# Kernel optimization log

Measured on AMD Instinct MI355X. Metric: run time of the kernel, lower is better.

Reference implementation:

```python
import jax, jax.numpy as jnp
import numpy as np

# Model config (matches init_kwargs)
D_MODEL = 1536
NUM_HEADS = 16
QUERY_GROUPS = 4
HEAD_DIM = D_MODEL // NUM_HEADS  # 96
HEADS_PER_GROUP = NUM_HEADS // QUERY_GROUPS
ROPE_THETA = 10000.0
B, T, GH, GW = 2, 16, 16, 16
S = GH * GW  # spatial patches per frame
QKV_OUT = NUM_HEADS * HEAD_DIM + 2 * QUERY_GROUPS * HEAD_DIM  # 2304


def setup_inputs() -> dict:
    key = jax.random.key(0)
    k1, k2, k3 = jax.random.split(key, 3)
    x = jax.random.normal(k1, (B, T, S, D_MODEL), dtype=jnp.float32)
    padding_mask = jnp.ones((B * T, S), dtype=jnp.int32)
    # nn.Linear weights stored as [out, in]; y = x @ W.T
    w_qkv = jax.random.normal(k2, (QKV_OUT, D_MODEL), dtype=jnp.float32) * (1.0 / np.sqrt(D_MODEL))
    w_o = jax.random.normal(k3, (D_MODEL, D_MODEL), dtype=jnp.float32) * (1.0 / np.sqrt(D_MODEL))
    return {"x": x, "padding_mask": padding_mask, "w_qkv": w_qkv, "w_o": w_o}


def _rot_half(seg, cos, sin):
    # seg: [..., d]; half-split rotary rotation
    d = seg.shape[-1] // 2
    x1, x2 = seg[..., :d], seg[..., d:]
    return jnp.concatenate([x1 * cos - x2 * sin, x1 * sin + x2 * cos], axis=-1)


def _cos_sin(pos, seg_dim):
    # pos: [L] -> cos/sin [L, seg_dim//2]
    inv_freq = 1.0 / (ROPE_THETA ** (jnp.arange(seg_dim // 2, dtype=jnp.float32) * 2.0 / seg_dim))
    ang = pos.astype(jnp.float32)[:, None] * inv_freq[None, :]
    return jnp.cos(ang), jnp.sin(ang)


def _apply_rope3d(x):
    # x: [B*T, S, heads, HEAD_DIM]; head_dim split equally over (t, h, w) axes
    seg = HEAD_DIM // 3  # 32
    t_pos = jnp.tile(jnp.arange(T), B)            # [B*T] temporal index per attention-batch row
    h_pos = jnp.repeat(jnp.arange(GH), GW)        # [S]
    w_pos = jnp.tile(jnp.arange(GW), GH)          # [S]
    ct, st = _cos_sin(t_pos, seg)  # [B*T, seg/2]
    ch, sh = _cos_sin(h_pos, seg)  # [S, seg/2]
    cw, sw = _cos_sin(w_pos, seg)
    xt = _rot_half(x[..., :seg], ct[:, None, None, :], st[:, None, None, :])
    xh = _rot_half(x[..., seg:2 * seg], ch[None, :, None, :], sh[None, :, None, :])
    xw = _rot_half(x[..., 2 * seg:], cw[None, :, None, :], sw[None, :, None, :])
    return jnp.concatenate([xt, xh, xw], axis=-1)


def reference(x, padding_mask, w_qkv, w_o):
    # Spatial attention mode: [B, T, S, D] -> [B*T, S, D]
    xs = x.reshape(B * T, S, D_MODEL)
    qkv = jnp.einsum('bsd,od->bso', xs, w_qkv)  # [B*T, S, QKV_OUT]
    q_end = NUM_HEADS * HEAD_DIM
    k_end = q_end + QUERY_GROUPS * HEAD_DIM
    q = qkv[..., :q_end].reshape(B * T, S, NUM_HEADS, HEAD_DIM)
    k = qkv[..., q_end:k_end].reshape(B * T, S, QUERY_GROUPS, HEAD_DIM)
    v = qkv[..., k_end:].reshape(B * T, S, QUERY_GROUPS, HEAD_DIM)
    # RoPE3D on q and k
    q = _apply_rope3d(q)
    k = _apply_rope3d(k)
    # GQA: extend kv heads to num_heads (repeat_interleave)
    k = jnp.repeat(k, HEADS_PER_GROUP, axis=2)  # [B*T, S, NUM_HEADS, HEAD_DIM]
    v = jnp.repeat(v, HEADS_PER_GROUP, axis=2)
    scale = 1.0 / np.sqrt(HEAD_DIM)
    scores = jnp.einsum('bqhd,bkhd->bhqk', q, k) * scale  # [B*T, H, S, S]
    mask = (padding_mask != 0)[:, None, None, :]  # [B*T, 1, 1, S], True = attend
    scores = jnp.where(mask, scores, jnp.float32(-1e9))
    probs = jax.nn.softmax(scores, axis=-1)
    attn = jnp.einsum('bhqk,bkhd->bqhd', probs, v).reshape(B * T, S, D_MODEL)
    out = jnp.einsum('bsd,od->bso', attn, w_o)
    return out.reshape(B, T, S, D_MODEL)
```

## Files before the change

kernel.cpp:

```cpp
#include <hip/hip_runtime.h>
#include <hip/hip_bf16.h>
#include <stdint.h>

typedef __attribute__((ext_vector_type(8))) short short8;
typedef __attribute__((ext_vector_type(4))) float f32x4;
typedef __attribute__((ext_vector_type(4))) float f4;
typedef __attribute__((ext_vector_type(4))) short s4;

typedef __attribute__((address_space(1))) const void gvoid_t;
typedef __attribute__((address_space(3))) void lvoid_t;

__device__ __forceinline__ void gload_lds16(const void* g, void* l) {
  __builtin_amdgcn_global_load_lds((gvoid_t*)g, (lvoid_t*)l, 16, 0, 0);
}

__device__ __forceinline__ ushort f2b(float f) {
  union { float f; uint32_t u; } v; v.f = f;
  return (ushort)((v.u + 0x7fffu + ((v.u >> 16) & 1u)) >> 16);
}
__device__ __forceinline__ float b2f(ushort b) {
  union { uint32_t u; float f; } v; v.u = ((uint32_t)b) << 16;
  return v.f;
}

template <int N> __device__ __forceinline__ void wait_vmcnt();
template <> __device__ __forceinline__ void wait_vmcnt<0>() { asm volatile("s_waitcnt vmcnt(0)" ::: "memory"); }

__device__ __forceinline__ void wait_lgkm0() {
  asm volatile("s_waitcnt lgkmcnt(0)" ::: "memory");
  __builtin_amdgcn_sched_barrier(0);
}
__device__ __forceinline__ void barrier_fence() {
  asm volatile("s_barrier" ::: "memory");
}

__global__ void prep_kernel(const float* __restrict__ x, const float* __restrict__ wq,
                            const float* __restrict__ wo,
                            ushort* __restrict__ Xb, ushort* __restrict__ Wq,
                            ushort* __restrict__ Wo, float2* __restrict__ tab) {
  int b = blockIdx.x, tid = threadIdx.x;
  const float* in; ushort* out; int i;
  if (b < 12288)      { in = x;  out = Xb; i = b * 256 + tid; }
  else if (b < 15744) { in = wq; out = Wq; i = (b - 12288) * 256 + tid; }
  else if (b < 18048) { in = wo; out = Wo; i = (b - 15744) * 256 + tid; }
  else {
    int pos = tid >> 4, fi = tid & 15;
    float inv_freq = __expf(-(float)fi * 0.5756462732485115f);
    float ang = (float)pos * inv_freq;
    float sn, c;
    __sincosf(ang, &sn, &c);
    tab[tid] = make_float2(c, sn);
    return;
  }
  f4 v = ((const f4*)in)[i];
  s4 o;
  o.x = (short)f2b(v.x); o.y = (short)f2b(v.y);
  o.z = (short)f2b(v.z); o.w = (short)f2b(v.w);
  ((s4*)out)[i] = o;
}

template <int BN, typename OutT>
__global__ __launch_bounds__(512, 2) void gemm6(const ushort* __restrict__ A,
                                                const ushort* __restrict__ B,
                                                OutT* __restrict__ C,
                                                int N, int K) {
  constexpr int NF = BN / 32;
  constexpr int RB = BN / 2;
  constexpr int ABUF = 256 * 64;
  constexpr int BBUF = BN * 64;
  constexpr uint ABYTE = ABUF * 2;
  constexpr uint BBYTE = BBUF * 2;
  constexpr int BRND = BN / 64;
  constexpr int BTW = (BN % 64) / 8;

  __shared__ ushort As[2 * ABUF];
  __shared__ ushort Bs[2 * BBUF];

  const int tid = threadIdx.x;
  const int l = tid & 63, w = tid >> 6;
  const int wr = w >> 1, wc = w & 1;
  const int r16 = l & 15, kh = l >> 4;
  const int sc = (l & 7) ^ (l >> 3);
  const int srow = w * 8 + (l >> 3);

  const int xcd = blockIdx.x & 7;
  const int ii = blockIdx.x >> 3;
  const int bm = xcd * 4 + (ii & 3);
  const int bn = ii >> 2;
  const ushort* Ag = A + (size_t)bm * 256 * K;
  const ushort* Bg = B + (size_t)bn * BN * K;
  const int NT = K >> 6;

  const char* AsR = (const char*)As;
  const char* BsR = (const char*)Bs;
  const uint khsw = ((uint)kh * 16) ^ ((uint)(r16 & 7) * 16);
  const uint PA = (uint)(wr * 64 + r16) * 128 + khsw;
  const uint PB = (uint)(wc * RB + r16) * 128 + khsw;

  const ushort* ga[4];
  const ushort* gb[BRND];
  const ushort* gbt = nullptr;
#pragma unroll
  for (int i = 0; i < 4; ++i) ga[i] = Ag + (size_t)(i * 64 + srow) * K + sc * 8;
#pragma unroll
  for (int i = 0; i < BRND; ++i) gb[i] = Bg + (size_t)(i * 64 + srow) * K + sc * 8;
  if constexpr (BTW > 0) gbt = Bg + (size_t)(BRND * 64 + srow) * K + sc * 8;

#pragma unroll
  for (int i = 0; i < 4; ++i) gload_lds16(ga[i], As + i * 4096 + w * 512);
#pragma unroll
  for (int i = 0; i < BRND; ++i) gload_lds16(gb[i], Bs + i * 4096 + w * 512);
  if constexpr (BTW > 0) { if (w < BTW) gload_lds16(gbt, Bs + BRND * 4096 + w * 512); }
#pragma unroll
  for (int i = 0; i < 4; ++i) ga[i] += 64;
#pragma unroll
  for (int i = 0; i < BRND; ++i) gb[i] += 64;
  if constexpr (BTW > 0) gbt += 64;
  wait_vmcnt<0>();
  barrier_fence();

  f32x4 acc[4][NF] = {};
  short8 afr[4], bfr[NF];

  for (int u = 0; u < NT; ++u) {
    const int cur = u & 1;
    const uint aoff = cur ? ABYTE : 0u;
    const uint boff = cur ? BBYTE : 0u;
    ushort* An = As + (cur ^ 1) * ABUF;
    ushort* Bn = Bs + (cur ^ 1) * BBUF;
    const bool st = (u + 1 < NT);

    {
      const uint pa = PA + aoff, pb = PB + boff;
#pragma unroll
      for (int m = 0; m < 4; ++m) afr[m] = *(const short8*)(AsR + pa + m * 2048);
#pragma unroll
      for (int n = 0; n < NF; ++n) bfr[n] = *(const short8*)(BsR + pb + n * 2048);
    }
    if (st) {
#pragma unroll
      for (int i = 0; i < 4; ++i) gload_lds16(ga[i], An + i * 4096 + w * 512);
    }
    wait_lgkm0();
    __builtin_amdgcn_s_setprio(1);
#pragma unroll
    for (int m = 0; m < 4; ++m)
#pragma unroll
      for (int n = 0; n < NF; ++n)
        acc[m][n] = __builtin_amdgcn_mfma_f32_16x16x32_bf16(afr[m], bfr[n], acc[m][n], 0, 0, 0);
    __builtin_amdgcn_s_setprio(0);

    {
      const uint pa = (PA ^ 64u) + aoff, pb = (PB ^ 64u) + boff;
#pragma unroll
      for (int m = 0; m < 4; ++m) afr[m] = *(const short8*)(AsR + pa + m * 2048);
#pragma unroll
      for (int n = 0; n < NF; ++n) bfr[n] = *(const short8*)(BsR + pb + n * 2048);
    }
    if (st) {
#pragma unroll
      for (int i = 0; i < BRND; ++i) gload_lds16(gb[i], Bn + i * 4096 + w * 512);
      if constexpr (BTW > 0) { if (w < BTW) gload_lds16(gbt, Bn + BRND * 4096 + w * 512); }
    }
    wait_lgkm0();
    __builtin_amdgcn_s_setprio(1);
#pragma unroll
    for (int m = 0; m < 4; ++m)
#pragma unroll
      for (int n = 0; n < NF; ++n)
        acc[m][n] = __builtin_amdgcn_mfma_f32_16x16x32_bf16(afr[m], bfr[n], acc[m][n], 0, 0, 0);
    __builtin_amdgcn_s_setprio(0);

#pragma unroll
    for (int i = 0; i < 4; ++i) ga[i] += 64;
#pragma unroll
    for (int i = 0; i < BRND; ++i) gb[i] += 64;
    if constexpr (BTW > 0) gbt += 64;
    wait_vmcnt<0>();
    barrier_fence();
  }

  const int rowb = bm * 256 + wr * 64;
  const int colb = bn * BN + wc * RB;
#pragma unroll
  for (int m = 0; m < 4; ++m)
#pragma unroll
    for (int n = 0; n < NF; ++n)
#pragma unroll
      for (int r = 0; r < 4; ++r) {
        int row = rowb + m * 16 + kh * 4 + r;
        int col = colb + n * 16 + r16;
        float val = acc[m][n][r];
        if constexpr (sizeof(OutT) == 2) C[(size_t)row * N + col] = f2b(val);
        else                             C[(size_t)row * N + col] = val;
      }
}

template <int BN, int KC, typename OutT>
__global__ __launch_bounds__(256, 2) void gemm12(const ushort* __restrict__ A,
                                                 const ushort* __restrict__ B,
                                                 OutT* __restrict__ C) {
  constexpr int NF = BN / 32;
  constexpr int RB = BN / 2;
  constexpr int ABUF = 128 * 64;
  constexpr int BBUF = BN * 64;
  constexpr uint ABYTE = ABUF * 2;
  constexpr uint BBYTE = BBUF * 2;
  constexpr int ARND = 4;
  constexpr int BRND = BN / 32;
  constexpr int NT = KC >> 6;

  __shared__ ushort As[2 * ABUF];
  __shared__ ushort Bs[2 * BBUF];

  const int tid = threadIdx.x;
  const int l = tid & 63, w = tid >> 6;
  const int wr = w >> 1, wc = w & 1;
  const int r16 = l & 15, kh = l >> 4;
  const int sc = (l & 7) ^ (l >> 3);
  const int srow = w * 8 + (l >> 3);

  const int xcd = blockIdx.x & 7;
  const int ii = blockIdx.x >> 3;
  const int bm = xcd * 8 + (ii & 7);
  const int bn = ii >> 3;
  const ushort* Ag = A + (size_t)bm * 128 * KC;
  const ushort* Bg = B + (size_t)bn * BN * KC;

  const char* AsR = (const char*)As;
  const char* BsR = (const char*)Bs;
  const uint khsw = ((uint)kh * 16) ^ ((uint)(r16 & 7) * 16);
  const uint PA = (uint)(wr * 64 + r16) * 128 + khsw;
  const uint PB = (uint)(wc * RB + r16) * 128 + khsw;

  const ushort* gA = Ag + (size_t)srow * KC + sc * 8;
  const ushort* gB = Bg + (size_t)srow * KC + sc * 8;

#pragma unroll
  for (int i = 0; i < ARND; ++i) gload_lds16(gA + (size_t)(i * 32) * KC, As + i * 2048 + w * 512);
#pragma unroll
  for (int i = 0; i < BRND; ++i) gload_lds16(gB + (size_t)(i * 32) * KC, Bs + i * 2048 + w * 512);
  gA += 64; gB += 64;
  wait_vmcnt<0>();
  barrier_fence();

  f32x4 acc[4][NF] = {};
  short8 afr[4], bfr[NF];

  for (int u = 0; u < NT; ++u) {
    const int cur = u & 1;
    const uint aoff = cur ? ABYTE : 0u;
    const uint boff = cur ? BBYTE : 0u;
    ushort* An = As + (cur ^ 1) * ABUF;
    ushort* Bn = Bs + (cur ^ 1) * BBUF;
    const bool st = (u + 1 < NT);

    {
      const uint pa = PA + aoff, pb = PB + boff;
#pragma unroll
      for (int m = 0; m < 4; ++m) afr[m] = *(const short8*)(AsR + pa + m * 2048);
#pragma unroll
      for (int n = 0; n < NF; ++n) bfr[n] = *(const short8*)(BsR + pb + n * 2048);
    }
    if (st) {
#pragma unroll
      for (int i = 0; i < ARND; ++i) gload_lds16(gA + (size_t)(i * 32) * KC, An + i * 2048 + w * 512);
    }
    wait_lgkm0();
    __builtin_amdgcn_s_setprio(1);
#pragma unroll
    for (int m = 0; m < 4; ++m)
#pragma unroll
      for (int n = 0; n < NF; ++n)
        acc[m][n] = __builtin_amdgcn_mfma_f32_16x16x32_bf16(afr[m], bfr[n], acc[m][n], 0, 0, 0);
    __builtin_amdgcn_s_setprio(0);

    {
      const uint pa = (PA ^ 64u) + aoff, pb = (PB ^ 64u) + boff;
#pragma unroll
      for (int m = 0; m < 4; ++m) afr[m] = *(const short8*)(AsR + pa + m * 2048);
#pragma unroll
      for (int n = 0; n < NF; ++n) bfr[n] = *(const short8*)(BsR + pb + n * 2048);
    }
    if (st) {
#pragma unroll
      for (int i = 0; i < BRND; ++i) gload_lds16(gB + (size_t)(i * 32) * KC, Bn + i * 2048 + w * 512);
    }
    wait_lgkm0();
    __builtin_amdgcn_s_setprio(1);
#pragma unroll
    for (int m = 0; m < 4; ++m)
#pragma unroll
      for (int n = 0; n < NF; ++n)
        acc[m][n] = __builtin_amdgcn_mfma_f32_16x16x32_bf16(afr[m], bfr[n], acc[m][n], 0, 0, 0);
    __builtin_amdgcn_s_setprio(0);

    gA += 64; gB += 64;
    wait_vmcnt<0>();
    barrier_fence();
  }

  const int rowb = bm * 128 + wr * 64;
  const int colb = bn * BN + wc * RB;
#pragma unroll
  for (int m = 0; m < 4; ++m)
#pragma unroll
    for (int n = 0; n < NF; ++n)
#pragma unroll
      for (int r = 0; r < 4; ++r) {
        int row = rowb + m * 16 + kh * 4 + r;
        int col = colb + n * 16 + r16;
        float val = acc[m][n][r];
        if constexpr (sizeof(OutT) == 2) C[(size_t)row * (BN * 8) + col] = f2b(val);
        else                             C[(size_t)row * (BN * 8) + col] = val;
      }
}

__device__ __forceinline__ short8 shfl_xor32(short8 v) {
  union { short8 s; int i[4]; } a, b;
  a.s = v;
#pragma unroll
  for (int q = 0; q < 4; ++q) b.i[q] = __shfl_xor(a.i[q], 32, 64);
  return b.s;
}
__device__ __forceinline__ short8 rope_frag(short8 v, int pos, int kh, const float2* Tb) {
  short8 p = shfl_xor32(v);
  const float sgn = (kh < 2) ? -1.0f : 1.0f;
  const int ib = pos * 16 + (kh & 1) * 8;
  short8 o;
#pragma unroll
  for (int j = 0; j < 8; ++j) {
    float2 cs = Tb[ib + j];
    o[j] = (short)f2b(b2f((ushort)v[j]) * cs.x + sgn * b2f((ushort)p[j]) * cs.y);
  }
  return o;
}

__global__ __launch_bounds__(512, 1) void attn3_kernel(
    const ushort* __restrict__ QKV,
    const int* __restrict__ mask,
    const float2* __restrict__ Tab,
    ushort* __restrict__ Out) {
  __shared__ ushort Ks[256 * 104];
  __shared__ ushort Vs[96 * 264];
  __shared__ ushort Ps[8][16 * 136];
  __shared__ float Mb[256];
  __shared__ float2 Tb[256];

  const int b = blockIdx.x;
  const int qt = b & 1;
  const int g = (b >> 1) & 3;
  const int bt = b >> 3;
  const int t = threadIdx.x;
  const int l = t & 63, w = t >> 6;
  const int r16 = l & 15, kh = l >> 4;
  const int h = g * 4 + (w >> 1);
  const int qc = w & 1;
  const int t0 = bt & 15;

  if (t < 256) { Tb[t] = Tab[t]; Mb[t] = mask[bt * 256 + t] ? 0.0f : -1.0e9f; }
  __syncthreads();

  {
    const int r = t >> 1, ch = t & 1;
    const ushort* src = QKV + (size_t)(bt * 256 + r) * 2304 + 1536 + g * 96;
    const int p1 = r >> 4, p2 = r & 15;
    if (ch == 0) {
      short8 v0 = *(const short8*)(src + 0);
      short8 v1 = *(const short8*)(src + 8);
      short8 v2 = *(const short8*)(src + 16);
      short8 v3 = *(const short8*)(src + 24);
      short8 o0, o1, o2, o3;
#pragma unroll
      for (int j = 0; j < 8; ++j) {
        float2 ca = Tb[t0 * 16 + j], cb = Tb[t0 * 16 + 8 + j];
        float x1a = b2f((ushort)v0[j]), x2a = b2f((ushort)v2[j]);
        float x1b = b2f((ushort)v1[j]), x2b = b2f((ushort)v3[j]);
        o0[j] = (short)f2b(x1a * ca.x - x2a * ca.y);
        o1[j] = (short)f2b(x1b * cb.x - x2b * cb.y);
        o2[j] = (short)f2b(x1a * ca.y + x2a * ca.x);
        o3[j] = (short)f2b(x1b * cb.y + x2b * cb.x);
      }
      *(short8*)(&Ks[r * 104 + 0])  = o0;
      *(short8*)(&Ks[r * 104 + 8])  = o1;
      *(short8*)(&Ks[r * 104 + 16]) = o2;
      *(short8*)(&Ks[r * 104 + 24]) = o3;
      v0 = *(const short8*)(src + 32);
      v1 = *(const short8*)(src + 40);
      v2 = *(const short8*)(src + 48);
      v3 = *(const short8*)(src + 56);
#pragma unroll
      for (int j = 0; j < 8; ++j) {
        float2 ca = Tb[p1 * 16 + j], cb = Tb[p1 * 16 + 8 + j];
        float x1a = b2f((ushort)v0[j]), x2a = b2f((ushort)v2[j]);
        float x1b = b2f((ushort)v1[j]), x2b = b2f((ushort)v3[j]);
        o0[j] = (short)f2b(x1a * ca.x - x2a * ca.y);
        o1[j] = (short)f2b(x1b * cb.x - x2b * cb.y);
        o2[j] = (short)f2b(x1a * ca.y + x2a * ca.x);
        o3[j] = (short)f2b(x1b * cb.y + x2b * cb.x);
      }
      *(short8*)(&Ks[r * 104 + 32]) = o0;
      *(short8*)(&Ks[r * 104 + 40]) = o1;
      *(short8*)(&Ks[r * 104 + 48]) = o2;
      *(short8*)(&Ks[r * 104 + 56]) = o3;
    } else {
      short8 v0 = *(const short8*)(src + 64);
      short8 v1 = *(const short8*)(src + 72);
      short8 v2 = *(const short8*)(src + 80);
      short8 v3 = *(const short8*)(src + 88);
      short8 o0, o1, o2, o3;
#pragma unroll
      for (int j = 0; j < 8; ++j) {
        float2 ca = Tb[p2 * 16 + j], cb = Tb[p2 * 16 + 8 + j];
        float x1a = b2f((ushort)v0[j]), x2a = b2f((ushort)v2[j]);
        float x1b = b2f((ushort)v1[j]), x2b = b2f((ushort)v3[j]);
        o0[j] = (short)f2b(x1a * ca.x - x2a * ca.y);
        o1[j] = (short)f2b(x1b * cb.x - x2b * cb.y);
        o2[j] = (short)f2b(x1a * ca.y + x2a * ca.x);
        o3[j] = (short)f2b(x1b * cb.y + x2b * cb.x);
      }
      *(short8*)(&Ks[r * 104 + 64]) = o0;
      *(short8*)(&Ks[r * 104 + 72]) = o1;
      *(short8*)(&Ks[r * 104 + 80]) = o2;
      *(short8*)(&Ks[r * 104 + 88]) = o3;
    }
  }

#pragma unroll
  for (int i = 0; i < 6; ++i) {
    int c = t + i * 512;
    int s = c / 12, dq = c - s * 12;
    short8 vv = *(const short8*)(QKV + (size_t)(bt * 256 + s) * 2304 + 1920 + g * 96 + dq * 8);
#pragma unroll
    for (int j = 0; j < 8; ++j)
      Vs[(dq * 8 + j) * 264 + s] = (ushort)vv[j];
  }
  __syncthreads();

  const ushort* Qp = QKV + (size_t)(bt * 256 + qt * 128 + qc * 64) * 2304 + h * 96;
  ushort* Pw = &Ps[w][0];
  const float scale = 0.10206207261596575f;

#pragma unroll
  for (int mp = 0; mp < 2; ++mp) {
    const int qb = mp * 32;
    const int p1A = qt * 8 + qc * 4 + mp * 2;
    const int p1B = p1A + 1;

    short8 qfA[3], qfB[3];
    {
      short8 rA0 = *(const short8*)(Qp + (size_t)(qb + r16) * 2304 + 0 + kh * 8);
      short8 rA1 = *(const short8*)(Qp + (size_t)(qb + r16) * 2304 + 32 + kh * 8);
      short8 rA2 = *(const short8*)(Qp + (size_t)(qb + r16) * 2304 + 64 + kh * 8);
      short8 rB0 = *(const short8*)(Qp + (size_t)(qb + 16 + r16) * 2304 + 0 + kh * 8);
      short8 rB1 = *(const short8*)(Qp + (size_t)(qb + 16 + r16) * 2304 + 32 + kh * 8);
      short8 rB2 = *(const short8*)(Qp + (size_t)(qb + 16 + r16) * 2304 + 64 + kh * 8);
      qfA[0] = rope_frag(rA0, t0, kh, Tb);
      qfA[1] = rope_frag(rA1, p1A, kh, Tb);
      qfA[2] = rope_frag(rA2, r16, kh, Tb);
      qfB[0] = rope_frag(rB0, t0, kh, Tb);
      qfB[1] = rope_frag(rB1, p1B, kh, Tb);
      qfB[2] = rope_frag(rB2, r16, kh, Tb);
    }

    f32x4 scA[16] = {}, scB[16] = {};
#pragma unroll
    for (int f = 0; f < 16; ++f) {
#pragma unroll
      for (int kc = 0; kc < 3; ++kc) {
        short8 kf = *(const short8*)(&Ks[(f * 16 + r16) * 104 + kc * 32 + kh * 8]);
        scA[f] = __builtin_amdgcn_mfma_f32_16x16x32_bf16(qfA[kc], kf, scA[f], 0, 0, 0);
        scB[f] = __builtin_amdgcn_mfma_f32_16x16x32_bf16(qfB[kc], kf, scB[f], 0, 0, 0);
      }
    }

#pragma unroll
    for (int f = 0; f < 16; ++f) {
      float mb = Mb[f * 16 + r16];
#pragma unroll
      for (int r = 0; r < 4; ++r) {
        scA[f][r] = scA[f][r] * scale + mb;
        scB[f][r] = scB[f][r] * scale + mb;
      }
    }

    float invA[4], invB[4];
#pragma unroll
    for (int reg = 0; reg < 4; ++reg) {
      float mxA = -3.0e38f, mxB = -3.0e38f;
#pragma unroll
      for (int f = 0; f < 16; ++f) { mxA = fmaxf(mxA, scA[f][reg]); mxB = fmaxf(mxB, scB[f][reg]); }
      for (int o = 8; o >= 1; o >>= 1) { mxA = fmaxf(mxA, __shfl_xor(mxA, o, 64)); mxB = fmaxf(mxB, __shfl_xor(mxB, o, 64)); }
      float smA = 0.f, smB = 0.f;
#pragma unroll
      for (int f = 0; f < 16; ++f) {
        float pA = __expf(scA[f][reg] - mxA);
        float pB = __expf(scB[f][reg] - mxB);
        scA[f][reg] = pA; scB[f][reg] = pB;
        smA += pA; smB += pB;
      }
      for (int o = 8; o >= 1; o >>= 1) { smA += __shfl_xor(smA, o, 64); smB += __shfl_xor(smB, o, 64); }
      invA[reg] = 1.0f / smA;
      invB[reg] = 1.0f / smB;
    }

    short8 pfA[8], pfB[8];
#pragma unroll
    for (int ck = 0; ck < 2; ++ck) {
#pragma unroll
      for (int f = 0; f < 8; ++f)
#pragma unroll
        for (int reg = 0; reg < 4; ++reg)
          Pw[(kh * 4 + reg) * 136 + f * 16 + r16] = f2b(scA[ck * 8 + f][reg]);
#pragma unroll
      for (int kc = 0; kc < 4; ++kc)
        pfA[ck * 4 + kc] = *(const short8*)(&Pw[r16 * 136 + kc * 32 + kh * 8]);
    }
#pragma unroll
    for (int ck = 0; ck < 2; ++ck) {
#pragma unroll
      for (int f = 0; f < 8; ++f)
#pragma unroll
        for (int reg = 0; reg < 4; ++reg)
          Pw[(kh * 4 + reg) * 136 + f * 16 + r16] = f2b(scB[ck * 8 + f][reg]);
#pragma unroll
      for (int kc = 0; kc < 4; ++kc)
        pfB[ck * 4 + kc] = *(const short8*)(&Pw[r16 * 136 + kc * 32 + kh * 8]);
    }

    f32x4 oA[6] = {}, oB[6] = {};
#pragma unroll
    for (int dt = 0; dt < 6; ++dt) {
#pragma unroll
      for (int kc = 0; kc < 8; ++kc) {
        short8 vf = *(const short8*)(&Vs[(dt * 16 + r16) * 264 + kc * 32 + kh * 8]);
        oA[dt] = __builtin_amdgcn_mfma_f32_16x16x32_bf16(pfA[kc], vf, oA[dt], 0, 0, 0);
        oB[dt] = __builtin_amdgcn_mfma_f32_16x16x32_bf16(pfB[kc], vf, oB[dt], 0, 0, 0);
      }
    }

    const int rbase = bt * 256 + qt * 128 + qc * 64 + qb;
#pragma unroll
    for (int dt = 0; dt < 6; ++dt)
#pragma unroll
      for (int reg = 0; reg < 4; ++reg) {
        int col = h * 96 + dt * 16 + r16;
        Out[(size_t)(rbase + kh * 4 + reg) * 1536 + col]      = f2b(oA[dt][reg] * invA[reg]);
        Out[(size_t)(rbase + 16 + kh * 4 + reg) * 1536 + col] = f2b(oB[dt][reg] * invB[reg]);
      }
  }
}

extern "C" void kernel_launch(void* const* d_in, const int* in_sizes, int n_in,
                              void* d_out, int out_size, void* d_ws, size_t ws_size,
                              hipStream_t stream) {
  const float* x     = (const float*)d_in[0];
  const int* pmask   = (const int*)d_in[1];
  const float* w_qkv = (const float*)d_in[2];
  const float* w_o   = (const float*)d_in[3];
  float* out = (float*)d_out;

  char* ws = (char*)d_ws;
  ushort* Xb  = (ushort*)(ws + 0);
  ushort* Wq  = (ushort*)(ws + 25165824);
  ushort* Wo  = (ushort*)(ws + 32243712);
  ushort* QKV = (ushort*)(ws + 36962304);
  float2* Tab = (float2*)(ws + 74711040);
  ushort* Attn = Xb;

  prep_kernel<<<18049, 256, 0, stream>>>(x, w_qkv, w_o, Xb, Wq, Wo, Tab);

  gemm6<288, ushort><<<256, 512, 0, stream>>>(Xb, Wq, QKV, 2304, 1536);

  attn3_kernel<<<256, 512, 0, stream>>>(QKV, pmask, Tab, Attn);

  gemm12<192, 1536, float><<<512, 256, 0, stream>>>(Attn, Wo, out);
}
```

Measured before the change: 147.5 us.

## Fuse fp32-to-bf16 conversion of x into the QKV GEMM's A-tile loads

The QKV projection GEMM now reads the fp32 activations directly, converts them to bf16 in registers with packed conversion instructions, and writes them to LDS. This replaces the separate pass that wrote a bf16 copy of x. The goal is to remove the extra read and write of the 25 MB activation buffer, at the cost of register-staged A loads instead of async global-to-LDS loads. Separately, the output projection switches from gemm12 to gemm6 with BN=192 and 512-thread blocks, and the workspace layout is rearranged.

```diff
diff --git a/kernel.cpp b/kernel.cpp
--- a/kernel.cpp
+++ b/kernel.cpp
@@ -6,6 +6,7 @@
 typedef __attribute__((ext_vector_type(4))) float f32x4;
 typedef __attribute__((ext_vector_type(4))) float f4;
 typedef __attribute__((ext_vector_type(4))) short s4;
+typedef __attribute__((ext_vector_type(4))) uint u4;
 
 typedef __attribute__((address_space(1))) const void gvoid_t;
 typedef __attribute__((address_space(3))) void lvoid_t;
@@ -22,6 +23,11 @@
   union { uint32_t u; float f; } v; v.u = ((uint32_t)b) << 16;
   return v.f;
 }
+__device__ __forceinline__ uint cvtpk(float lo, float hi) {
+  uint r;
+  asm volatile("v_cvt_pk_bf16_f32 %0, %1, %2" : "=v"(r) : "v"(lo), "v"(hi));
+  return r;
+}
 
 template <int N> __device__ __forceinline__ void wait_vmcnt();
 template <> __device__ __forceinline__ void wait_vmcnt<0>() { asm volatile("s_waitcnt vmcnt(0)" ::: "memory"); }
@@ -34,15 +40,13 @@
   asm volatile("s_barrier" ::: "memory");
 }
 
-__global__ void prep_kernel(const float* __restrict__ x, const float* __restrict__ wq,
-                            const float* __restrict__ wo,
-                            ushort* __restrict__ Xb, ushort* __restrict__ Wq,
-                            ushort* __restrict__ Wo, float2* __restrict__ tab) {
+__global__ void prep2_kernel(const float* __restrict__ wq, const float* __restrict__ wo,
+                             ushort* __restrict__ Wq, ushort* __restrict__ Wo,
+                             float2* __restrict__ tab) {
   int b = blockIdx.x, tid = threadIdx.x;
   const float* in; ushort* out; int i;
-  if (b < 12288)      { in = x;  out = Xb; i = b * 256 + tid; }
-  else if (b < 15744) { in = wq; out = Wq; i = (b - 12288) * 256 + tid; }
-  else if (b < 18048) { in = wo; out = Wo; i = (b - 15744) * 256 + tid; }
+  if (b < 3456)      { in = wq; out = Wq; i = b * 256 + tid; }
+  else if (b < 5760) { in = wo; out = Wo; i = (b - 3456) * 256 + tid; }
   else {
     int pos = tid >> 4, fi = tid & 15;
     float inv_freq = __expf(-(float)fi * 0.5756462732485115f);
@@ -57,6 +61,165 @@
   o.x = (short)f2b(v.x); o.y = (short)f2b(v.y);
   o.z = (short)f2b(v.z); o.w = (short)f2b(v.w);
   ((s4*)out)[i] = o;
+}
+
+__global__ __launch_bounds__(512, 2) void gemm6x(const float* __restrict__ Af,
+                                                 const ushort* __restrict__ B,
+                                                 ushort* __restrict__ C) {
+  constexpr int BN = 288, NF = 9, RB = 144;
+  constexpr int K = 1536, NT = 24;
+  constexpr int ABUF = 256 * 64;
+  constexpr int BBUF = BN * 64;
+  constexpr uint ABYTE = ABUF * 2;
+  constexpr uint BBYTE = BBUF * 2;
+  constexpr int BRND = 4, BTW = 4;
+
+  __shared__ ushort As[2 * ABUF];
+  __shared__ ushort Bs[2 * BBUF];
+
+  const int tid = threadIdx.x;
+  const int l = tid & 63, w = tid >> 6;
+  const int wr = w >> 1, wc = w & 1;
+  const int r16 = l & 15, kh = l >> 4;
+  const int sc = (l & 7) ^ (l >> 3);
+  const int srow = w * 8 + (l >> 3);
+
+  const int xcd = blockIdx.x & 7;
+  const int ii = blockIdx.x >> 3;
+  const int bm = xcd * 4 + (ii & 3);
+  const int bn = ii >> 2;
+  const float* Ag = Af + (size_t)bm * 256 * K;
+  const ushort* Bg = B + (size_t)bn * BN * K;
+
+  const char* AsR = (const char*)As;
+  const char* BsR = (const char*)Bs;
+  const uint khsw = ((uint)kh * 16) ^ ((uint)(r16 & 7) * 16);
+  const uint PA = (uint)(wr * 64 + r16) * 128 + khsw;
+  const uint PB = (uint)(wc * RB + r16) * 128 + khsw;
+
+  const float* gaf[4];
+  const ushort* gb[BRND];
+  const ushort* gbt;
+#pragma unroll
+  for (int i = 0; i < 4; ++i) gaf[i] = Ag + (size_t)(i * 64 + srow) * K + sc * 8;
+#pragma unroll
+  for (int i = 0; i < BRND; ++i) gb[i] = Bg + (size_t)(i * 64 + srow) * K + sc * 8;
+  gbt = Bg + (size_t)(BRND * 64 + srow) * K + sc * 8;
+
+  const uint adst = (uint)w * 512 + (uint)l * 8;
+
+  {
+    f4 p0[4], p1[4];
+#pragma unroll
+    for (int i = 0; i < 4; ++i) {
+      p0[i] = *((const f4*)gaf[i]);
+      p1[i] = *((const f4*)gaf[i] + 1);
+    }
+#pragma unroll
+    for (int i = 0; i < 4; ++i) {
+      u4 pk;
+      pk.x = cvtpk(p0[i].x, p0[i].y);
+      pk.y = cvtpk(p0[i].z, p0[i].w);
+      pk.z = cvtpk(p1[i].x, p1[i].y);
+      pk.w = cvtpk(p1[i].z, p1[i].w);
+      *(u4*)(&As[i * 4096 + adst]) = pk;
+    }
+  }
+#pragma unroll
+  for (int i = 0; i < BRND; ++i) gload_lds16(gb[i], Bs + i * 4096 + w * 512);
+  if (w < BTW) gload_lds16(gbt, Bs + BRND * 4096 + w * 512);
+#pragma unroll
+  for (int i = 0; i < BRND; ++i) gb[i] += 64;
+  gbt += 64;
+  wait_vmcnt<0>();
+  wait_lgkm0();
+  barrier_fence();
+
+  f32x4 acc[4][NF] = {};
+  short8 afr[4], bfr[NF];
+  f4 a0[4], a1[4];
+
+  for (int u = 0; u < NT; ++u) {
+    const int cur = u & 1;
+    const uint aoff = cur ? ABYTE : 0u;
+    const uint boff = cur ? BBYTE : 0u;
+    ushort* An = As + (cur ^ 1) * ABUF;
+    ushort* Bn = Bs + (cur ^ 1) * BBUF;
+    const bool st = (u + 1 < NT);
+    const int kt1 = (u + 1) * 64;
+
+    {
+      const uint pa = PA + aoff, pb = PB + boff;
+#pragma unroll
+      for (int m = 0; m < 4; ++m) afr[m] = *(const short8*)(AsR + pa + m * 2048);
+#pragma unroll
+      for (int n = 0; n < NF; ++n) bfr[n] = *(const short8*)(BsR + pb + n * 2048);
+    }
+    if (st) {
+#pragma unroll
+      for (int i = 0; i < 4; ++i) {
+        a0[i] = *((const f4*)(gaf[i] + kt1));
+        a1[i] = *((const f4*)(gaf[i] + kt1) + 1);
+      }
+    }
+    wait_lgkm0();
+    __builtin_amdgcn_s_setprio(1);
+#pragma unroll
+    for (int m = 0; m < 4; ++m)
+#pragma unroll
+      for (int n = 0; n < NF; ++n)
+        acc[m][n] = __builtin_amdgcn_mfma_f32_16x16x32_bf16(afr[m], bfr[n], acc[m][n], 0, 0, 0);
+    __builtin_amdgcn_s_setprio(0);
+
+    {
+      const uint pa = (PA ^ 64u) + aoff, pb = (PB ^ 64u) + boff;
+#pragma unroll
+      for (int m = 0; m < 4; ++m) afr[m] = *(const short8*)(AsR + pa + m * 2048);
+#pragma unroll
+      for (int n = 0; n < NF; ++n) bfr[n] = *(const short8*)(BsR + pb + n * 2048);
+    }
+    if (st) {
+#pragma unroll
+      for (int i = 0; i < 4; ++i) {
+        u4 pk;
+        pk.x = cvtpk(a0[i].x, a0[i].y);
+        pk.y = cvtpk(a0[i].z, a0[i].w);
+        pk.z = cvtpk(a1[i].x, a1[i].y);
+        pk.w = cvtpk(a1[i].z, a1[i].w);
+        *(u4*)(&An[i * 4096 + adst]) = pk;
+      }
+#pragma unroll
+      for (int i = 0; i < BRND; ++i) gload_lds16(gb[i], Bn + i * 4096 + w * 512);
+      if (w < BTW) gload_lds16(gbt, Bn + BRND * 4096 + w * 512);
+#pragma unroll
+      for (int i = 0; i < BRND; ++i) gb[i] += 64;
+      gbt += 64;
+    }
+    wait_lgkm0();
+    __builtin_amdgcn_s_setprio(1);
+#pragma unroll
+    for (int m = 0; m < 4; ++m)
+#pragma unroll
+      for (int n = 0; n < NF; ++n)
+        acc[m][n] = __builtin_amdgcn_mfma_f32_16x16x32_bf16(afr[m], bfr[n], acc[m][n], 0, 0, 0);
+    __builtin_amdgcn_s_setprio(0);
+
+    wait_vmcnt<0>();
+    barrier_fence();
+  }
+
+  const int rowb = bm * 256 + wr * 64;
+  const int colb = bn * BN + wc * RB;
+#pragma unroll
+  for (int m = 0; m < 4; ++m)
+#pragma unroll
+    for (int n = 0; n < NF; ++n)
+#pragma unroll
+      for (int r = 0; r < 4; ++r) {
+        int row = rowb + m * 16 + kh * 4 + r;
+        int col = colb + n * 16 + r16;
+        C[(size_t)row * 2304 + col] = f2b(acc[m][n][r]);
+      }
 }
 
 template <int BN, typename OutT>
@@ -193,126 +356,6 @@
         float val = acc[m][n][r];
         if constexpr (sizeof(OutT) == 2) C[(size_t)row * N + col] = f2b(val);
         else                             C[(size_t)row * N + col] = val;
-      }
-}
-
-template <int BN, int KC, typename OutT>
-__global__ __launch_bounds__(256, 2) void gemm12(const ushort* __restrict__ A,
-                                                 const ushort* __restrict__ B,
-                                                 OutT* __restrict__ C) {
-  constexpr int NF = BN / 32;
-  constexpr int RB = BN / 2;
-  constexpr int ABUF = 128 * 64;
-  constexpr int BBUF = BN * 64;
-  constexpr uint ABYTE = ABUF * 2;
-  constexpr uint BBYTE = BBUF * 2;
-  constexpr int ARND = 4;
-  constexpr int BRND = BN / 32;
-  constexpr int NT = KC >> 6;
-
-  __shared__ ushort As[2 * ABUF];
-  __shared__ ushort Bs[2 * BBUF];
-
-  const int tid = threadIdx.x;
-  const int l = tid & 63, w = tid >> 6;
-  const int wr = w >> 1, wc = w & 1;
-  const int r16 = l & 15, kh = l >> 4;
-  const int sc = (l & 7) ^ (l >> 3);
-  const int srow = w * 8 + (l >> 3);
-
-  const int xcd = blockIdx.x & 7;
-  const int ii = blockIdx.x >> 3;
-  const int bm = xcd * 8 + (ii & 7);
-  const int bn = ii >> 3;
-  const ushort* Ag = A + (size_t)bm * 128 * KC;
-  const ushort* Bg = B + (size_t)bn * BN * KC;
-
-  const char* AsR = (const char*)As;
-  const char* BsR = (const char*)Bs;
-  const uint khsw = ((uint)kh * 16) ^ ((uint)(r16 & 7) * 16);
-  const uint PA = (uint)(wr * 64 + r16) * 128 + khsw;
-  const uint PB = (uint)(wc * RB + r16) * 128 + khsw;
-
-  const ushort* gA = Ag + (size_t)srow * KC + sc * 8;
-  const ushort* gB = Bg + (size_t)srow * KC + sc * 8;
-
-#pragma unroll
-  for (int i = 0; i < ARND; ++i) gload_lds16(gA + (size_t)(i * 32) * KC, As + i * 2048 + w * 512);
-#pragma unroll
-  for (int i = 0; i < BRND; ++i) gload_lds16(gB + (size_t)(i * 32) * KC, Bs + i * 2048 + w * 512);
-  gA += 64; gB += 64;
-  wait_vmcnt<0>();
-  barrier_fence();
-
-  f32x4 acc[4][NF] = {};
-  short8 afr[4], bfr[NF];
-
-  for (int u = 0; u < NT; ++u) {
-    const int cur = u & 1;
-    const uint aoff = cur ? ABYTE : 0u;
-    const uint boff = cur ? BBYTE : 0u;
-    ushort* An = As + (cur ^ 1) * ABUF;
-    ushort* Bn = Bs + (cur ^ 1) * BBUF;
-    const bool st = (u + 1 < NT);
-
-    {
-      const uint pa = PA + aoff, pb = PB + boff;
-#pragma unroll
-      for (int m = 0; m < 4; ++m) afr[m] = *(const short8*)(AsR + pa + m * 2048);
-#pragma unroll
-      for (int n = 0; n < NF; ++n) bfr[n] = *(const short8*)(BsR + pb + n * 2048);
-    }
-    if (st) {
-#pragma unroll
-      for (int i = 0; i < ARND; ++i) gload_lds16(gA + (size_t)(i * 32) * KC, An + i * 2048 + w * 512);
-    }
-    wait_lgkm0();
-    __builtin_amdgcn_s_setprio(1);
-#pragma unroll
-    for (int m = 0; m < 4; ++m)
-#pragma unroll
-      for (int n = 0; n < NF; ++n)
-        acc[m][n] = __builtin_amdgcn_mfma_f32_16x16x32_bf16(afr[m], bfr[n], acc[m][n], 0, 0, 0);
-    __builtin_amdgcn_s_setprio(0);
-
-    {
-      const uint pa = (PA ^ 64u) + aoff, pb = (PB ^ 64u) + boff;
-#pragma unroll
-      for (int m = 0; m < 4; ++m) afr[m] = *(const short8*)(AsR + pa + m * 2048);
-#pragma unroll
-      for (int n = 0; n < NF; ++n) bfr[n] = *(const short8*)(BsR + pb + n * 2048);
-    }
-    if (st) {
-#pragma unroll
-      for (int i = 0; i < BRND; ++i) gload_lds16(gB + (size_t)(i * 32) * KC, Bn + i * 2048 + w * 512);
-    }
-    wait_lgkm0();
-    __builtin_amdgcn_s_setprio(1);
-#pragma unroll
-    for (int m = 0; m < 4; ++m)
-#pragma unroll
-      for (int n = 0; n < NF; ++n)
-        acc[m][n] = __builtin_amdgcn_mfma_f32_16x16x32_bf16(afr[m], bfr[n], acc[m][n], 0, 0, 0);
-    __builtin_amdgcn_s_setprio(0);
-
-    gA += 64; gB += 64;
-    wait_vmcnt<0>();
-    barrier_fence();
-  }
-
-  const int rowb = bm * 128 + wr * 64;
-  const int colb = bn * BN + wc * RB;
-#pragma unroll
-  for (int m = 0; m < 4; ++m)
-#pragma unroll
-    for (int n = 0; n < NF; ++n)
-#pragma unroll
-      for (int r = 0; r < 4; ++r) {
-        int row = rowb + m * 16 + kh * 4 + r;
-        int col = colb + n * 16 + r16;
-        float val = acc[m][n][r];
-        if constexpr (sizeof(OutT) == 2) C[(size_t)row * (BN * 8) + col] = f2b(val);
-        else                             C[(size_t)row * (BN * 8) + col] = val;
       }
 }
 
@@ -561,18 +604,17 @@
   float* out = (float*)d_out;
 
   char* ws = (char*)d_ws;
-  ushort* Xb  = (ushort*)(ws + 0);
-  ushort* Wq  = (ushort*)(ws + 25165824);
-  ushort* Wo  = (ushort*)(ws + 32243712);
-  ushort* QKV = (ushort*)(ws + 36962304);
-  float2* Tab = (float2*)(ws + 74711040);
-  ushort* Attn = Xb;
-
-  prep_kernel<<<18049, 256, 0, stream>>>(x, w_qkv, w_o, Xb, Wq, Wo, Tab);
-
-  gemm6<288, ushort><<<256, 512, 0, stream>>>(Xb, Wq, QKV, 2304, 1536);
+  ushort* Wq   = (ushort*)(ws + 0);
+  ushort* Wo   = (ushort*)(ws + 7077888);
+  ushort* QKV  = (ushort*)(ws + 11796480);
+  float2* Tab  = (float2*)(ws + 49545216);
+  ushort* Attn = (ushort*)(ws + 49547264);
+
+  prep2_kernel<<<5761, 256, 0, stream>>>(w_qkv, w_o, Wq, Wo, Tab);
+
+  gemm6x<<<256, 512, 0, stream>>>(x, Wq, QKV);
 
   attn3_kernel<<<256, 512, 0, stream>>>(QKV, pmask, Tab, Attn);
 
-  gemm12<192, 1536, float><<<512, 256, 0, stream>>>(Attn, Wo, out);
-}
+  gemm6<192, float><<<256, 512, 0, stream>>>(Attn, Wo, out, 1536, 1536);
+}
```

After: 144.4 us (median of 2 runs). 1.02x faster.
